# Performance work log

Measured on AMD Instinct MI355X. Metric: run time of the kernel, lower is better.

Reference implementation:

```python
import jax, jax.numpy as jnp
import numpy as np

N = 40000
E = 640000
D_IN = 128
H = 8
C = 16  # out_dim per head


def setup_inputs() -> dict:
    key = jax.random.key(0)
    ks = jax.random.split(key, 7)
    features = jax.random.normal(ks[0], (N, D_IN), dtype=jnp.float32)
    edge_index = jax.random.randint(ks[1], (2, E), 0, N, dtype=jnp.int32)
    edge_weight = jax.random.uniform(ks[2], (E,), dtype=jnp.float32)
    # xavier-ish scales
    W_lin = jax.random.normal(ks[3], (D_IN, H * C), dtype=jnp.float32) * (1.0 / np.sqrt(D_IN))
    att_l = jax.random.normal(ks[4], (1, H, C), dtype=jnp.float32) * 0.1
    att_r = jax.random.normal(ks[5], (1, H, C), dtype=jnp.float32) * 0.1
    W_res = jax.random.normal(ks[6], (D_IN, H * C), dtype=jnp.float32) * (1.0 / np.sqrt(D_IN))
    return {"features": features, "edge_index": edge_index, "edge_weight": edge_weight,
            "W_lin": W_lin, "att_l": att_l, "att_r": att_r, "W_res": W_res}


def _segment_softmax(logits, seg, num_segments):
    # logits: (E, H), seg: (E,) destination node ids
    m = jax.ops.segment_max(logits, seg, num_segments=num_segments)  # (N, H)
    ex = jnp.exp(logits - m[seg])
    s = jax.ops.segment_sum(ex, seg, num_segments=num_segments)  # (N, H)
    return ex / s[seg]


def reference(features, edge_index, edge_weight, W_lin, att_l, att_r, W_res):
    src, dst = edge_index[0], edge_index[1]
    x = (features @ W_lin).reshape(-1, H, C)              # (N, H, C)
    alpha_l = (x * att_l).sum(-1)                          # (N, H)
    alpha_r = (x * att_r).sum(-1)                          # (N, H)
    alpha = alpha_l[src] + alpha_r[dst]                    # (E, H)
    alpha = edge_weight[:, None] * alpha
    alpha = jnp.where(alpha >= 0, alpha, 0.2 * alpha)      # leaky_relu(0.2)
    coef = _segment_softmax(alpha, dst, N)                 # (E, H)
    msgs = x[src] * coef[:, :, None]                       # (E, H, C)
    agg = jax.ops.segment_sum(msgs, dst, num_segments=N)   # (N, H, C)
    out = jax.nn.elu(agg).reshape(-1, H * C)
    out = out + features @ W_res
    return out
```

## Files before the change

kernel.cpp:

```cpp
#include <hip/hip_runtime.h>
#include <math.h>

#define N_NODES 40000
#define N_EDGES 640000
#define D 128
#define H 8
#define C 16
#define NBG 1250
#define KP 136
#define NBUCK 2500
#define NCH 512
#define ECH 1250
#define CAP 4
#define SLOTS_B (NCH * CAP)
#define MAXB 384
#define OVCAP 4096
#define SOVC 64

typedef __attribute__((ext_vector_type(8))) short short8;
typedef __attribute__((ext_vector_type(4))) float floatx4;


__device__ __forceinline__ unsigned short f2bf(float f) {
  const unsigned u = __float_as_uint(f);
  return (unsigned short)((u + 0x7FFFu + ((u >> 16) & 1u)) >> 16);
}
__device__ __forceinline__ float bflo(unsigned p) {
  return __uint_as_float(p << 16);
}
__device__ __forceinline__ float bfhi(unsigned p) {
  return __uint_as_float(p & 0xFFFF0000u);
}
__device__ __forceinline__ float bf2f(unsigned short u) {
  return __uint_as_float((unsigned)u << 16);
}

__global__ void k_prep(const float* __restrict__ Wlin,
                       const float* __restrict__ Wres,
                       unsigned short* __restrict__ wt, int* __restrict__ ovfn)
{
  const int n = blockIdx.x, k = threadIdx.x, g = blockIdx.y;
  if (n == 0 && g == 0 && k == 0) *ovfn = 0;
  const float* W = g ? Wres : Wlin;
  wt[((g * 128 + n) * 128) + k] = f2bf(W[(long)k * 128 + n]);
}

__global__ __launch_bounds__(256, 4) void k_gemm(
    const float* __restrict__ feat, const unsigned short* __restrict__ wt,
    unsigned short* __restrict__ xh, float* __restrict__ outp,
    const float* __restrict__ attl, const float* __restrict__ attr,
    float* __restrict__ al, float* __restrict__ ar,
    const int* __restrict__ src, const int* __restrict__ dst,
    const float* __restrict__ ew, uint2* __restrict__ einfo,
    int* __restrict__ cnt2, int* __restrict__ ovfn, uint4* __restrict__ ovf)
{
  __shared__ short sA[32 * KP];
  __shared__ float sD[32 * 132];
  const int t = threadIdx.x;

  if (blockIdx.y == 1) {
    if (blockIdx.x >= NCH) return;
    int* lcnt = (int*)sD;
    for (int i = t; i < NBUCK; i += 256) lcnt[i] = 0;
    __syncthreads();
    const int c = blockIdx.x;
    const int e0 = c * ECH;
    for (int e = e0 + t; e < e0 + ECH; e += 256) {
      const int d = dst[e];
      const int b = d >> 4, dl = d & 15;
      const int r = atomicAdd(&lcnt[b], 1);
      const unsigned pay = ((unsigned)src[e] << 4) | (unsigned)dl;
      const unsigned wbits = __float_as_uint(ew[e]);
      if (r < CAP) {
        einfo[((long)b * NCH + c) * CAP + r] = make_uint2(pay, wbits);
      } else {
        const int oi = atomicAdd(ovfn, 1);
        if (oi < OVCAP)
          ovf[oi] = make_uint4((unsigned)b, (unsigned)dl,
                               (unsigned)src[e], wbits);
      }
    }
    __syncthreads();
    for (int i = t; i < NBUCK; i += 256) cnt2[c * NBUCK + i] = lcnt[i];
    return;
  }

  const int row0 = blockIdx.x * 32;

  {
    const int kq = t & 31;
    const int rb = (t >> 5) * 4;
    #pragma unroll
    for (int i = 0; i < 4; ++i) {
      const int r = rb + i;
      const float4 f = *(const float4*)&feat[(long)(row0 + r) * 128 + kq * 4];
      const unsigned lo = (unsigned)f2bf(f.x) | ((unsigned)f2bf(f.y) << 16);
      const unsigned hi = (unsigned)f2bf(f.z) | ((unsigned)f2bf(f.w) << 16);
      *(uint2*)&sA[r * KP + kq * 4] = make_uint2(lo, hi);
    }
  }

  const int w = t >> 6, lane = t & 63;
  const int c15 = lane & 15, q = lane >> 4;

  short8 bfr0[4][2], bfr1[4][2];
  #pragma unroll
  for (int kc = 0; kc < 4; ++kc)
    #pragma unroll
    for (int nt = 0; nt < 2; ++nt) {
      const int n = (w * 2 + nt) * 16 + c15;
      bfr0[kc][nt] = *(const short8*)&wt[n * 128 + kc * 32 + q * 8];
      bfr1[kc][nt] = *(const short8*)&wt[16384 + n * 128 + kc * 32 + q * 8];
    }
  __syncthreads();

  floatx4 acc0[2][2], acc1[2][2];
  #pragma unroll
  for (int mt = 0; mt < 2; ++mt)
    #pragma unroll
    for (int nt = 0; nt < 2; ++nt) {
      acc0[mt][nt] = (floatx4){0.f, 0.f, 0.f, 0.f};
      acc1[mt][nt] = (floatx4){0.f, 0.f, 0.f, 0.f};
    }
  #pragma unroll
  for (int kc = 0; kc < 4; ++kc)
    #pragma unroll
    for (int mt = 0; mt < 2; ++mt) {
      const short8 afr = *(const short8*)&sA[(mt * 16 + c15) * KP + kc * 32 + q * 8];
      acc0[mt][0] = __builtin_amdgcn_mfma_f32_16x16x32_bf16(afr, bfr0[kc][0], acc0[mt][0], 0, 0, 0);
      acc0[mt][1] = __builtin_amdgcn_mfma_f32_16x16x32_bf16(afr, bfr0[kc][1], acc0[mt][1], 0, 0, 0);
      acc1[mt][0] = __builtin_amdgcn_mfma_f32_16x16x32_bf16(afr, bfr1[kc][0], acc1[mt][0], 0, 0, 0);
      acc1[mt][1] = __builtin_amdgcn_mfma_f32_16x16x32_bf16(afr, bfr1[kc][1], acc1[mt][1], 0, 0, 0);
    }

  const int orow = t >> 3, seg = t & 7;
  const int grow = row0 + orow;

  #pragma unroll
  for (int mt = 0; mt < 2; ++mt)
    #pragma unroll
    for (int nt = 0; nt < 2; ++nt) {
      const int col = (w * 2 + nt) * 16 + c15;
      #pragma unroll
      for (int r = 0; r < 4; ++r)
        sD[(mt * 16 + q * 4 + r) * 132 + col] = acc0[mt][nt][r];
    }
  __syncthreads();
  {
    #pragma unroll
    for (int i = 0; i < 2; ++i) {
      const float4 v0 = *(const float4*)&sD[orow * 132 + seg * 16 + i * 8];
      const float4 v1 = *(const float4*)&sD[orow * 132 + seg * 16 + i * 8 + 4];
      uint4 u;
      u.x = (unsigned)f2bf(v0.x) | ((unsigned)f2bf(v0.y) << 16);
      u.y = (unsigned)f2bf(v0.z) | ((unsigned)f2bf(v0.w) << 16);
      u.z = (unsigned)f2bf(v1.x) | ((unsigned)f2bf(v1.y) << 16);
      u.w = (unsigned)f2bf(v1.z) | ((unsigned)f2bf(v1.w) << 16);
      *(uint4*)&xh[(long)grow * 128 + seg * 16 + i * 8] = u;
    }
    const int h = seg;
    float sl = 0.f, sr = 0.f;
    #pragma unroll
    for (int c4 = 0; c4 < 4; ++c4) {
      const float4 xv = *(const float4*)&sD[orow * 132 + h * 16 + c4 * 4];
      const float4 lv = *(const float4*)&attl[h * 16 + c4 * 4];
      const float4 rv = *(const float4*)&attr[h * 16 + c4 * 4];
      sl += xv.x * lv.x + xv.y * lv.y + xv.z * lv.z + xv.w * lv.w;
      sr += xv.x * rv.x + xv.y * rv.y + xv.z * rv.z + xv.w * rv.w;
    }
    al[(long)grow * 8 + h] = sl;
    ar[(long)grow * 8 + h] = sr;
  }
  __syncthreads();

  #pragma unroll
  for (int mt = 0; mt < 2; ++mt)
    #pragma unroll
    for (int nt = 0; nt < 2; ++nt) {
      const int col = (w * 2 + nt) * 16 + c15;
      #pragma unroll
      for (int r = 0; r < 4; ++r)
        sD[(mt * 16 + q * 4 + r) * 132 + col] = acc1[mt][nt][r];
    }
  __syncthreads();
  #pragma unroll
  for (int i = 0; i < 4; ++i) {
    const float4 v = *(const float4*)&sD[orow * 132 + seg * 16 + i * 4];
    *(float4*)&outp[(long)grow * 128 + seg * 16 + i * 4] = v;
  }
}

__global__ __launch_bounds__(256, 8) void k_edgeagg(
    const int* __restrict__ cnt2, const uint2* __restrict__ einfo,
    const int* __restrict__ ovfn, const uint4* __restrict__ ovf,
    const float* __restrict__ al, const float* __restrict__ ar,
    const unsigned short* __restrict__ xh, float* __restrict__ outp)
{
  __shared__ unsigned short sP[MAXB * 8];
  __shared__ int sS[MAXB];
  __shared__ float sAr[128];
  __shared__ int scnt[NCH];
  __shared__ uint2 sOv[SOVC];
  __shared__ int bcnt[16], bbase[16], bpos[16], nOv;
  const int b = blockIdx.x;
  const int t = threadIdx.x;
  if (t < 16) bcnt[t] = 0;
  if (t == 16) nOv = 0;
  if (t < 128) sAr[t] = ar[(long)(b << 4) * 8 + t];
  for (int i = t; i < NCH; i += 256)
    scnt[i] = min(cnt2[i * NBUCK + b], CAP);
  __syncthreads();

  const long base = (long)b * SLOTS_B;

  for (int i = t; i < SLOTS_B; i += 256) {
    const int c = i >> 2, r = i & 3;
    if (r < scnt[c]) {
      const uint2 m = einfo[base + i];
      atomicAdd(&bcnt[m.x & 15], 1);
    }
  }
  const int no = *ovfn;
  for (int i = t; i < no; i += 256) {
    const uint4 o = ovf[i];
    if ((int)o.x == b) {
      const int k = atomicAdd(&nOv, 1);
      if (k < SOVC) {
        sOv[k] = make_uint2((o.z << 4) | o.y, o.w);
        atomicAdd(&bcnt[o.y], 1);
      }
    }
  }
  __syncthreads();

  if (t < 16) {
    const int v = bcnt[t];
    int incl = v;
    #pragma unroll
    for (int off = 1; off < 16; off <<= 1) {
      const int n = __shfl_up(incl, off, 16);
      if (t >= off) incl += n;
    }
    bbase[t] = incl - v;
    bpos[t] = 0;
  }
  __syncthreads();

  auto process = [&](uint2 m) {
    const int dl = m.x & 15;
    const int s = (int)(m.x >> 4);
    const float w = __uint_as_float(m.y);
    const float4 l0 = *(const float4*)&al[(long)s * 8];
    const float4 l1 = *(const float4*)&al[(long)s * 8 + 4];
    const float* arr = &sAr[dl * 8];
    float lv[8] = {l0.x + arr[0], l0.y + arr[1], l0.z + arr[2], l0.w + arr[3],
                   l1.x + arr[4], l1.y + arr[5], l1.z + arr[6], l1.w + arr[7]};
    #pragma unroll
    for (int h = 0; h < 8; ++h) {
      float a = w * lv[h];
      a = (a >= 0.f) ? a : 0.2f * a;
      lv[h] = __expf(a);
    }
    const int r = atomicAdd(&bpos[dl], 1);
    const int qq = bbase[dl] + r;
    sS[qq] = s;
    uint4 u;
    u.x = (unsigned)f2bf(lv[0]) | ((unsigned)f2bf(lv[1]) << 16);
    u.y = (unsigned)f2bf(lv[2]) | ((unsigned)f2bf(lv[3]) << 16);
    u.z = (unsigned)f2bf(lv[4]) | ((unsigned)f2bf(lv[5]) << 16);
    u.w = (unsigned)f2bf(lv[6]) | ((unsigned)f2bf(lv[7]) << 16);
    *(uint4*)&sP[qq * 8] = u;
  };
  for (int i = t; i < SLOTS_B; i += 256) {
    const int c = i >> 2, r = i & 3;
    if (r < scnt[c]) process(einfo[base + i]);
  }
  const int nov = min(nOv, SOVC);
  for (int i = t; i < nov; i += 256) process(sOv[i]);
  __syncthreads();

  const int wv = t >> 6, lane = t & 63;
  const int h = lane >> 3;
  const int co = lane * 2;
  #pragma unroll
  for (int j = 0; j < 4; ++j) {
    const int dl = wv * 4 + j;
    const int start = bbase[dl];
    const int end = start + bcnt[dl];
    if (end <= start) continue;

    float2 a0 = {0.f, 0.f}, a1 = {0.f, 0.f}, a2 = {0.f, 0.f}, a3 = {0.f, 0.f};
    float s0s = 0.f, s1s = 0.f, s2s = 0.f, s3s = 0.f;
    int p = start;
    for (; p + 4 <= end; p += 4) {
      const int s0 = sS[p + 0], s1 = sS[p + 1];
      const int s2 = sS[p + 2], s3 = sS[p + 3];
      const float e0v = bf2f(sP[(p + 0) * 8 + h]);
      const float e1v = bf2f(sP[(p + 1) * 8 + h]);
      const float e2v = bf2f(sP[(p + 2) * 8 + h]);
      const float e3v = bf2f(sP[(p + 3) * 8 + h]);
      const unsigned v0 = *(const unsigned*)&xh[(long)s0 * 128 + co];
      const unsigned v1 = *(const unsigned*)&xh[(long)s1 * 128 + co];
      const unsigned v2 = *(const unsigned*)&xh[(long)s2 * 128 + co];
      const unsigned v3 = *(const unsigned*)&xh[(long)s3 * 128 + co];
      a0.x = fmaf(bflo(v0), e0v, a0.x); a0.y = fmaf(bfhi(v0), e0v, a0.y); s0s += e0v;
      a1.x = fmaf(bflo(v1), e1v, a1.x); a1.y = fmaf(bfhi(v1), e1v, a1.y); s1s += e1v;
      a2.x = fmaf(bflo(v2), e2v, a2.x); a2.y = fmaf(bfhi(v2), e2v, a2.y); s2s += e2v;
      a3.x = fmaf(bflo(v3), e3v, a3.x); a3.y = fmaf(bfhi(v3), e3v, a3.y); s3s += e3v;
    }
    for (; p < end; ++p) {
      const int s = sS[p];
      const float ev = bf2f(sP[p * 8 + h]);
      const unsigned v = *(const unsigned*)&xh[(long)s * 128 + co];
      a0.x = fmaf(bflo(v), ev, a0.x);
      a0.y = fmaf(bfhi(v), ev, a0.y);
      s0s += ev;
    }
    const float rs = 1.0f / ((s0s + s1s) + (s2s + s3s));
    const float ax = ((a0.x + a1.x) + (a2.x + a3.x)) * rs;
    const float ay = ((a0.y + a1.y) + (a2.y + a3.y)) * rs;

    const long dnode = (long)(b << 4) + dl;
    float2 o = *(float2*)&outp[dnode * 128 + co];
    o.x += (ax > 0.f) ? ax : expm1f(ax);
    o.y += (ay > 0.f) ? ay : expm1f(ay);
    *(float2*)&outp[dnode * 128 + co] = o;
  }
}

extern "C" void kernel_launch(void* const* d_in, const int* in_sizes, int n_in,
                              void* d_out, int out_size, void* d_ws, size_t ws_size,
                              hipStream_t stream) {
  const float* feat = (const float*)d_in[0];
  const int*   eidx = (const int*)d_in[1];
  const float* ew   = (const float*)d_in[2];
  const float* Wlin = (const float*)d_in[3];
  const float* attl = (const float*)d_in[4];
  const float* attr = (const float*)d_in[5];
  const float* Wres = (const float*)d_in[6];
  float* outp = (float*)d_out;

  float* ws = (float*)d_ws;
  unsigned short* xh = (unsigned short*)ws;
  float* al   = ws + 5120000;
  float* ar   = ws + 5440000;
  uint2* einfo = (uint2*)(ws + 6000000);
  int*   cnt2 = (int*)(ws + 16300000);
  int*   ovfn = (int*)(ws + 17600000);
  uint4* ovf  = (uint4*)(ws + 17600064);
  unsigned short* wt = (unsigned short*)(ws + 17700000);

  const int* src = eidx;
  const int* dst = eidx + N_EDGES;

  dim3 pgrid(128, 2);
  k_prep<<<pgrid, 128, 0, stream>>>(Wlin, Wres, wt, ovfn);
  dim3 ggrid(NBG, 2);
  k_gemm<<<ggrid, 256, 0, stream>>>(feat, wt, xh, outp, attl, attr, al, ar,
                                    src, dst, ew, einfo, cnt2, ovfn, ovf);
  k_edgeagg<<<NBUCK, 256, 0, stream>>>(cnt2, einfo, ovfn, ovf, al, ar,
                                       xh, outp);
}
```

Before: 165.5 us.

## Replace per-destination bucket sort with single append list in edge aggregation

Drops the counting pass, prefix scan and two block barriers that grouped edges by local destination. Each edge is now appended to one shared list tagged with its destination, and each wave scans the whole list, keeping only entries for its four destinations and routing them to one of four accumulators. This avoids reading einfo twice and the extra synchronisation, but every wave now walks all entries with divergent branches, and the unrolled independent gathers of the old loop are lost.

```diff
diff --git a/kernel.cpp b/kernel.cpp
--- a/kernel.cpp
+++ b/kernel.cpp
@@ -200,12 +200,10 @@
   __shared__ int sS[MAXB];
   __shared__ float sAr[128];
   __shared__ int scnt[NCH];
-  __shared__ uint2 sOv[SOVC];
-  __shared__ int bcnt[16], bbase[16], bpos[16], nOv;
+  __shared__ int nE;
   const int b = blockIdx.x;
   const int t = threadIdx.x;
-  if (t < 16) bcnt[t] = 0;
-  if (t == 16) nOv = 0;
+  if (t == 0) nE = 0;
   if (t < 128) sAr[t] = ar[(long)(b << 4) * 8 + t];
   for (int i = t; i < NCH; i += 256)
     scnt[i] = min(cnt2[i * NBUCK + b], CAP);
@@ -213,43 +211,10 @@
 
   const long base = (long)b * SLOTS_B;
 
-  for (int i = t; i < SLOTS_B; i += 256) {
-    const int c = i >> 2, r = i & 3;
-    if (r < scnt[c]) {
-      const uint2 m = einfo[base + i];
-      atomicAdd(&bcnt[m.x & 15], 1);
-    }
-  }
-  const int no = *ovfn;
-  for (int i = t; i < no; i += 256) {
-    const uint4 o = ovf[i];
-    if ((int)o.x == b) {
-      const int k = atomicAdd(&nOv, 1);
-      if (k < SOVC) {
-        sOv[k] = make_uint2((o.z << 4) | o.y, o.w);
-        atomicAdd(&bcnt[o.y], 1);
-      }
-    }
-  }
-  __syncthreads();
-
-  if (t < 16) {
-    const int v = bcnt[t];
-    int incl = v;
-    #pragma unroll
-    for (int off = 1; off < 16; off <<= 1) {
-      const int n = __shfl_up(incl, off, 16);
-      if (t >= off) incl += n;
-    }
-    bbase[t] = incl - v;
-    bpos[t] = 0;
-  }
-  __syncthreads();
-
-  auto process = [&](uint2 m) {
-    const int dl = m.x & 15;
-    const int s = (int)(m.x >> 4);
-    const float w = __uint_as_float(m.y);
+  auto process = [&](unsigned pay, unsigned wbits) {
+    const int dl = pay & 15;
+    const int s = (int)(pay >> 4);
+    const float w = __uint_as_float(wbits);
     const float4 l0 = *(const float4*)&al[(long)s * 8];
     const float4 l1 = *(const float4*)&al[(long)s * 8 + 4];
     const float* arr = &sAr[dl * 8];
@@ -261,71 +226,67 @@
       a = (a >= 0.f) ? a : 0.2f * a;
       lv[h] = __expf(a);
     }
-    const int r = atomicAdd(&bpos[dl], 1);
-    const int qq = bbase[dl] + r;
-    sS[qq] = s;
-    uint4 u;
-    u.x = (unsigned)f2bf(lv[0]) | ((unsigned)f2bf(lv[1]) << 16);
-    u.y = (unsigned)f2bf(lv[2]) | ((unsigned)f2bf(lv[3]) << 16);
-    u.z = (unsigned)f2bf(lv[4]) | ((unsigned)f2bf(lv[5]) << 16);
-    u.w = (unsigned)f2bf(lv[6]) | ((unsigned)f2bf(lv[7]) << 16);
-    *(uint4*)&sP[qq * 8] = u;
+    const int k = atomicAdd(&nE, 1);
+    if (k < MAXB) {
+      sS[k] = (dl << 16) | s;
+      uint4 u;
+      u.x = (unsigned)f2bf(lv[0]) | ((unsigned)f2bf(lv[1]) << 16);
+      u.y = (unsigned)f2bf(lv[2]) | ((unsigned)f2bf(lv[3]) << 16);
+      u.z = (unsigned)f2bf(lv[4]) | ((unsigned)f2bf(lv[5]) << 16);
+      u.w = (unsigned)f2bf(lv[6]) | ((unsigned)f2bf(lv[7]) << 16);
+      *(uint4*)&sP[k * 8] = u;
+    }
   };
   for (int i = t; i < SLOTS_B; i += 256) {
     const int c = i >> 2, r = i & 3;
-    if (r < scnt[c]) process(einfo[base + i]);
-  }
-  const int nov = min(nOv, SOVC);
-  for (int i = t; i < nov; i += 256) process(sOv[i]);
+    if (r < scnt[c]) {
+      const uint2 m = einfo[base + i];
+      process(m.x, m.y);
+    }
+  }
+  const int no = *ovfn;
+  for (int i = t; i < no; i += 256) {
+    const uint4 o = ovf[i];
+    if ((int)o.x == b) process((o.z << 4) | o.y, o.w);
+  }
   __syncthreads();
 
   const int wv = t >> 6, lane = t & 63;
   const int h = lane >> 3;
   const int co = lane * 2;
-  #pragma unroll
-  for (int j = 0; j < 4; ++j) {
-    const int dl = wv * 4 + j;
-    const int start = bbase[dl];
-    const int end = start + bcnt[dl];
-    if (end <= start) continue;
-
-    float2 a0 = {0.f, 0.f}, a1 = {0.f, 0.f}, a2 = {0.f, 0.f}, a3 = {0.f, 0.f};
-    float s0s = 0.f, s1s = 0.f, s2s = 0.f, s3s = 0.f;
-    int p = start;
-    for (; p + 4 <= end; p += 4) {
-      const int s0 = sS[p + 0], s1 = sS[p + 1];
-      const int s2 = sS[p + 2], s3 = sS[p + 3];
-      const float e0v = bf2f(sP[(p + 0) * 8 + h]);
-      const float e1v = bf2f(sP[(p + 1) * 8 + h]);
-      const float e2v = bf2f(sP[(p + 2) * 8 + h]);
-      const float e3v = bf2f(sP[(p + 3) * 8 + h]);
-      const unsigned v0 = *(const unsigned*)&xh[(long)s0 * 128 + co];
-      const unsigned v1 = *(const unsigned*)&xh[(long)s1 * 128 + co];
-      const unsigned v2 = *(const unsigned*)&xh[(long)s2 * 128 + co];
-      const unsigned v3 = *(const unsigned*)&xh[(long)s3 * 128 + co];
-      a0.x = fmaf(bflo(v0), e0v, a0.x); a0.y = fmaf(bfhi(v0), e0v, a0.y); s0s += e0v;
-      a1.x = fmaf(bflo(v1), e1v, a1.x); a1.y = fmaf(bfhi(v1), e1v, a1.y); s1s += e1v;
-      a2.x = fmaf(bflo(v2), e2v, a2.x); a2.y = fmaf(bfhi(v2), e2v, a2.y); s2s += e2v;
-      a3.x = fmaf(bflo(v3), e3v, a3.x); a3.y = fmaf(bfhi(v3), e3v, a3.y); s3s += e3v;
-    }
-    for (; p < end; ++p) {
-      const int s = sS[p];
-      const float ev = bf2f(sP[p * 8 + h]);
-      const unsigned v = *(const unsigned*)&xh[(long)s * 128 + co];
-      a0.x = fmaf(bflo(v), ev, a0.x);
-      a0.y = fmaf(bfhi(v), ev, a0.y);
-      s0s += ev;
-    }
-    const float rs = 1.0f / ((s0s + s1s) + (s2s + s3s));
-    const float ax = ((a0.x + a1.x) + (a2.x + a3.x)) * rs;
-    const float ay = ((a0.y + a1.y) + (a2.y + a3.y)) * rs;
-
-    const long dnode = (long)(b << 4) + dl;
+  const int nEv = min(nE, MAXB);
+
+  float2 aA = {0.f, 0.f}, aB = {0.f, 0.f}, aC = {0.f, 0.f}, aD = {0.f, 0.f};
+  float ssA = 0.f, ssB = 0.f, ssC = 0.f, ssD = 0.f;
+  for (int p = 0; p < nEv; ++p) {
+    const int rec = sS[p];
+    const int dl = rec >> 16;
+    if ((dl >> 2) != wv) continue;
+    const int s = rec & 0xFFFF;
+    const float ev = bf2f(sP[p * 8 + h]);
+    const unsigned v = *(const unsigned*)&xh[(long)s * 128 + co];
+    const float xl = bflo(v), xhv = bfhi(v);
+    const int j = dl & 3;
+    if (j == 0)      { aA.x = fmaf(xl, ev, aA.x); aA.y = fmaf(xhv, ev, aA.y); ssA += ev; }
+    else if (j == 1) { aB.x = fmaf(xl, ev, aB.x); aB.y = fmaf(xhv, ev, aB.y); ssB += ev; }
+    else if (j == 2) { aC.x = fmaf(xl, ev, aC.x); aC.y = fmaf(xhv, ev, aC.y); ssC += ev; }
+    else             { aD.x = fmaf(xl, ev, aD.x); aD.y = fmaf(xhv, ev, aD.y); ssD += ev; }
+  }
+
+  auto wout = [&](int j, float2 a, float ss) {
+    if (ss <= 0.f) return;
+    const float rs = 1.0f / ss;
+    const float ax = a.x * rs, ay = a.y * rs;
+    const long dnode = (long)(b << 4) + wv * 4 + j;
     float2 o = *(float2*)&outp[dnode * 128 + co];
     o.x += (ax > 0.f) ? ax : expm1f(ax);
     o.y += (ay > 0.f) ? ay : expm1f(ay);
     *(float2*)&outp[dnode * 128 + co] = o;
-  }
+  };
+  wout(0, aA, ssA);
+  wout(1, aB, ssB);
+  wout(2, aC, ssC);
+  wout(3, aD, ssD);
 }
 
 extern "C" void kernel_launch(void* const* d_in, const int* in_sizes, int n_in,
```

Measured after the change: 216.1 us. 30.5% more time.
